# Performance work log

Measured on AMD Instinct MI355X. Metric: run time of the kernel, lower is better.

## Reference

```python
import jax, jax.numpy as jnp
import numpy as np

EPS = 1e-6
SLOPE = 0.25  # nn.PReLU() default init, recreated each forward -> constant slope


def conv_norm(x, W, b, g, beta):
    # 1x1 conv: [B,C,T,F] x [O,C] -> [B,O,T,F]
    y = jnp.einsum('bctf,oc->botf', x, W) + b[None, :, None, None]
    # GroupNorm(num_groups=1): normalize over (C,T,F) per sample
    mu = jnp.mean(y, axis=(1, 2, 3), keepdims=True)
    var = jnp.var(y, axis=(1, 2, 3), keepdims=True)
    y = (y - mu) * jax.lax.rsqrt(var + EPS)
    y = y * g[None, :, None, None] + beta[None, :, None, None]
    # PReLU with constant slope 0.25
    return jnp.where(y >= 0, y, SLOPE * y)


def setup_inputs() -> dict:
    key = jax.random.key(0)
    ks = jax.random.split(key, 16)
    B, C, T, F = 2, 256, 512, 128
    N, H = 4, 64
    CN = C // N
    f32 = jnp.float32

    def w(k, shape, fan_in):
        return jax.random.normal(k, shape, f32) / np.sqrt(fan_in).astype(np.float32)

    return {
        'x': jax.random.normal(ks[0], (B, C, T, F), f32),
        'Wq': w(ks[1], (N, H, C), C), 'bq': jnp.zeros((N, H), f32),
        'gq': jnp.ones((N, H), f32), 'betaq': jnp.zeros((N, H), f32),
        'Wk': w(ks[2], (N, H, C), C), 'bk': jnp.zeros((N, H), f32),
        'gk': jnp.ones((N, H), f32), 'betak': jnp.zeros((N, H), f32),
        'Wv': w(ks[3], (N, CN, C), C), 'bv': jnp.zeros((N, CN), f32),
        'gv': jnp.ones((N, CN), f32), 'betav': jnp.zeros((N, CN), f32),
        'Wp': w(ks[4], (C, C), C), 'bp': jnp.zeros((C,), f32),
        'gp': jnp.ones((C,), f32), 'betap': jnp.zeros((C,), f32),
    }


def reference(x, Wq, bq, gq, betaq, Wk, bk, gk, betak, Wv, bv, gv, betav,
              Wp, bp, gp, betap):
    B, C, T, F = x.shape
    N = Wq.shape[0]
    CN = C // N

    branch = jax.vmap(conv_norm, in_axes=(None, 0, 0, 0, 0))  # over N heads

    def to_seq(y):
        # [N,B,H,T,F] -> transpose(1,2) in torch -> [N,B,T,H,F] -> flatten(2)
        return jnp.swapaxes(y, 2, 3).reshape(y.shape[0], y.shape[1], y.shape[3], -1)

    Q = to_seq(branch(x, Wq, bq, gq, betaq))  # [N,B,T,H*F]
    K = to_seq(branch(x, Wk, bk, gk, betak))  # [N,B,T,H*F]
    V = to_seq(branch(x, Wv, bv, gv, betav))  # [N,B,T,CN*F]

    scale = 1.0 / np.sqrt(Q.shape[-1]).astype(np.float32)
    attn = jax.nn.softmax(jnp.einsum('nbtd,nbsd->nbts', Q, K) * scale, axis=-1)
    Vo = jnp.einsum('nbts,nbsd->nbtd', attn, V)  # [N,B,T,CN*F]

    # exact replication of the original reshape chain (incl. (f,t) reinterpret)
    Vo = Vo.reshape(N * B, T, CN * F)
    Vo = jnp.swapaxes(Vo, 1, 2)                    # [N*B, CN*F, T]
    Vo = Vo.reshape(N, B, CN, T, F)
    Vo = jnp.swapaxes(Vo, 0, 1).reshape(B, C, T, F)

    out = conv_norm(Vo, Wp, bp, gp, betap)
    return out + x
```

## Files before the change

kernel.cpp:

```cpp
#include <hip/hip_runtime.h>
#include <cstddef>

typedef unsigned short u16;

typedef __bf16 bf16x8 __attribute__((ext_vector_type(8)));
typedef float  f32x4  __attribute__((ext_vector_type(4)));
typedef short  s16x8  __attribute__((ext_vector_type(8)));

__device__ __forceinline__ float us2f(u16 u){
  unsigned int w = ((unsigned int)u) << 16; float f; __builtin_memcpy(&f,&w,4); return f;
}
__device__ __forceinline__ u16 f2us(float f){
  unsigned int u; __builtin_memcpy(&u,&f,4);
  u = (u + 0x7FFFu + ((u>>16)&1u)) >> 16;
  return (u16)u;
}

__device__ __forceinline__ f32x4 mfma16(bf16x8 a, bf16x8 b, f32x4 c){
  return __builtin_amdgcn_mfma_f32_16x16x32_bf16(a, b, c, 0, 0, 0);
}
__device__ __forceinline__ ushort4 pack4(f32x4 a){
  ushort4 p; p.x=f2us(a[0]); p.y=f2us(a[1]); p.z=f2us(a[2]); p.w=f2us(a[3]); return p;
}

constexpr int CC=256, CT=512, CF=128, CD=8192, CTF=65536;
constexpr float EPSV = 1e-6f;
constexpr float SLOPEV = 0.25f;
constexpr float QSCALE = 0.011048543456039806f;

#define OW_Q 0
#define OB_Q 65536
#define OG_Q 65792
#define OBE_Q 66048
#define OW_K 66304
#define OB_K 131840
#define OG_K 132096
#define OBE_K 132352
#define OW_V 132608
#define OB_V 198144
#define OG_V 198400
#define OBE_V 198656
#define OW_P 198912
#define OB_P 264448
#define OG_P 264704
#define OBE_P 264960

__global__ void k_detect(const u16* gq_raw, int* flagp){
  if (threadIdx.x==0 && blockIdx.x==0) *flagp = (gq_raw[0]==0x3F80) ? 1 : 0;
}

__global__ __launch_bounds__(256) void k_prep(
    const void* p1,const void* p2,const void* p3,const void* p4,
    const void* p5,const void* p6,const void* p7,const void* p8,
    const void* p9,const void* p10,const void* p11,const void* p12,
    const void* p13,const void* p14,const void* p15,const void* p16,
    u16* dst, const int* flagp)
{
  const void* src; int size; int off;
  switch(blockIdx.y){
    case  0: src=p1;  size=65536; off=OW_Q;  break;
    case  1: src=p2;  size=256;   off=OB_Q;  break;
    case  2: src=p3;  size=256;   off=OG_Q;  break;
    case  3: src=p4;  size=256;   off=OBE_Q; break;
    case  4: src=p5;  size=65536; off=OW_K;  break;
    case  5: src=p6;  size=256;   off=OB_K;  break;
    case  6: src=p7;  size=256;   off=OG_K;  break;
    case  7: src=p8;  size=256;   off=OBE_K; break;
    case  8: src=p9;  size=65536; off=OW_V;  break;
    case  9: src=p10; size=256;   off=OB_V;  break;
    case 10: src=p11; size=256;   off=OG_V;  break;
    case 11: src=p12; size=256;   off=OBE_V; break;
    case 12: src=p13; size=65536; off=OW_P;  break;
    case 13: src=p14; size=256;   off=OB_P;  break;
    case 14: src=p15; size=256;   off=OG_P;  break;
    default: src=p16; size=256;   off=OBE_P; break;
  }
  int idx = blockIdx.x*256 + threadIdx.x;
  if (idx >= size) return;
  u16 v;
  if (*flagp) v = ((const u16*)src)[idx];
  else        v = f2us(((const float*)src)[idx]);
  dst[off+idx] = v;
}

__global__ __launch_bounds__(256) void k_conv(
    const void* x, const u16* wtsb,
    u16* qn, u16* kn, u16* vn,
    float* stats, const int* flagp, int n, int b0)
{
  const int tid = threadIdx.x;
  const int tf0 = blockIdx.x * 64;
  const int flag = *flagp;

  __shared__ __align__(16) u16 Xs[64][264];
  __shared__ float wred[3][4][2];

  {
    const int tfl = (tid & 31) * 2;
    const int cb  = (tid >> 5) * 4;
    if (flag){
      const u16* xq = (const u16*)x + (size_t)b0*CC*CTF + tf0 + tfl;
      #pragma unroll
      for (int p=0;p<8;p++){
        int c0 = p*32 + cb;
        u16 a0[4], a1[4];
        #pragma unroll
        for (int i=0;i<4;i++){
          ushort2 u = *(const ushort2*)&xq[(size_t)(c0+i)*CTF];
          a0[i]=u.x; a1[i]=u.y;
        }
        *(ushort4*)&Xs[tfl][c0]   = *(const ushort4*)a0;
        *(ushort4*)&Xs[tfl+1][c0] = *(const ushort4*)a1;
      }
    } else {
      const float* xq = (const float*)x + (size_t)b0*CC*CTF + tf0 + tfl;
      #pragma unroll
      for (int p=0;p<8;p++){
        int c0 = p*32 + cb;
        u16 a0[4], a1[4];
        #pragma unroll
        for (int i=0;i<4;i++){
          float2 u = *(const float2*)&xq[(size_t)(c0+i)*CTF];
          a0[i]=f2us(u.x); a1[i]=f2us(u.y);
        }
        *(ushort4*)&Xs[tfl][c0]   = *(const ushort4*)a0;
        *(ushort4*)&Xs[tfl+1][c0] = *(const ushort4*)a1;
      }
    }
  }
  __syncthreads();

  const int l  = tid & 63, w = tid >> 6;
  const int lr = l & 15,  kg = l >> 4;
  const int wy = w >> 1,  wx = w & 1;
  const u16* arow0 = &Xs[wy*32 + lr][8*kg];
  const u16* arow1 = &Xs[wy*32 + 16 + lr][8*kg];
  const int t  = tf0 >> 7;
  const int fb = (tf0 & 127) + wy*32 + 4*kg;
  const int o0 = wx*32 + lr;

  for (int br=0; br<3; ++br){
    const u16* W    = wtsb + (br==0?OW_Q: br==1?OW_K:OW_V) + n*64*256;
    const u16* bias = wtsb + (br==0?OB_Q: br==1?OB_K:OB_V) + n*64;
    u16* yo = (br==0? qn : (br==1? kn : vn));
    const u16* bp0 = W + o0*256 + 8*kg;
    const u16* bp1 = bp0 + 16*256;
    float bb0 = us2f(bias[o0]);
    float bb1 = us2f(bias[o0+16]);
    f32x4 acc00 = {bb0,bb0,bb0,bb0};
    f32x4 acc01 = {bb1,bb1,bb1,bb1};
    f32x4 acc10 = {bb0,bb0,bb0,bb0};
    f32x4 acc11 = {bb1,bb1,bb1,bb1};
    #pragma unroll
    for (int d=0; d<256; d+=32){
      bf16x8 a0 = *(const bf16x8*)(arow0 + d);
      bf16x8 a1 = *(const bf16x8*)(arow1 + d);
      bf16x8 b0 = *(const bf16x8*)(bp0 + d);
      bf16x8 b1 = *(const bf16x8*)(bp1 + d);
      acc00 = mfma16(a0,b0,acc00);
      acc01 = mfma16(a0,b1,acc01);
      acc10 = mfma16(a1,b0,acc10);
      acc11 = mfma16(a1,b1,acc11);
    }
    float s=0.f, s2=0.f;
    #pragma unroll
    for (int ii=0; ii<4; ++ii){
      float v;
      v=acc00[ii]; s+=v; s2+=v*v;
      v=acc01[ii]; s+=v; s2+=v*v;
      v=acc10[ii]; s+=v; s2+=v*v;
      v=acc11[ii]; s+=v; s2+=v*v;
    }
    #pragma unroll
    for (int m=1; m<64; m<<=1){ s += __shfl_xor(s,m); s2 += __shfl_xor(s2,m); }
    if (l==0){ wred[br][w][0]=s; wred[br][w][1]=s2; }
    const size_t ybase = (size_t)t*CD + fb;
    *(ushort4*)&yo[ybase + (size_t)o0*CF]           = pack4(acc00);
    *(ushort4*)&yo[ybase + (size_t)(o0+16)*CF]      = pack4(acc01);
    *(ushort4*)&yo[ybase + 16 + (size_t)o0*CF]      = pack4(acc10);
    *(ushort4*)&yo[ybase + 16 + (size_t)(o0+16)*CF] = pack4(acc11);
  }
  __syncthreads();
  if (tid < 3){
    float s  = wred[tid][0][0]+wred[tid][1][0]+wred[tid][2][0]+wred[tid][3][0];
    float s2 = wred[tid][0][1]+wred[tid][1][1]+wred[tid][2][1]+wred[tid][3][1];
    int g = tid*8 + n*2 + b0;
    atomicAdd(&stats[2*g],   s);
    atomicAdd(&stats[2*g+1], s2);
  }
}

__global__ __launch_bounds__(256) void k_norm(
    u16* q, u16* k, u16* v, const u16* wtsb,
    const float* stats, int n, int b0)
{
  const int br = blockIdx.y;
  u16* y = (br==0? q : (br==1? k : v));
  const u16* g  = wtsb + (br==0?OG_Q : br==1?OG_K :OG_V ) + n*64;
  const u16* be = wtsb + (br==0?OBE_Q: br==1?OBE_K:OBE_V) + n*64;
  size_t idx0 = ((size_t)blockIdx.x*256 + threadIdx.x)*8;
  int ch = (int)((idx0 >> 7) & 63);
  int grp = br*8 + n*2 + b0;
  float sm = stats[2*grp], sq = stats[2*grp+1];
  const float Minv = 1.0f/4194304.0f;
  float mean = sm*Minv;
  float var  = fmaxf(sq*Minv - mean*mean, 0.0f);
  float rs = rsqrtf(var + EPSV);
  float gg = us2f(g[ch]) * rs;
  float bb = us2f(be[ch]);
  float sc = (br==0)? QSCALE : 1.0f;
  ushort4 u0 = *(const ushort4*)&y[idx0];
  ushort4 u1 = *(const ushort4*)&y[idx0+4];
  float vals[8] = {us2f(u0.x),us2f(u0.y),us2f(u0.z),us2f(u0.w),
                   us2f(u1.x),us2f(u1.y),us2f(u1.z),us2f(u1.w)};
  #pragma unroll
  for (int j=0;j<8;j++){
    float t = (vals[j]-mean)*gg + bb;
    t = (t>=0.f)? t : SLOPEV*t;
    vals[j] = t*sc;
  }
  ushort4 o0, o1;
  o0.x=f2us(vals[0]); o0.y=f2us(vals[1]); o0.z=f2us(vals[2]); o0.w=f2us(vals[3]);
  o1.x=f2us(vals[4]); o1.y=f2us(vals[5]); o1.z=f2us(vals[6]); o1.w=f2us(vals[7]);
  *(ushort4*)&y[idx0]   = o0;
  *(ushort4*)&y[idx0+4] = o1;
}

__global__ __launch_bounds__(512) void k_qk(const u16* __restrict__ qm,
                                            const u16* __restrict__ km,
                                            float* __restrict__ S)
{
  const int tid = threadIdx.x;
  const int l   = tid & 63;
  const int w   = tid >> 6;
  const int lr  = l & 15;
  const int kg  = l >> 4;
  const int s0  = blockIdx.x*32;
  const int t0  = blockIdx.y*32;

  const u16* qp = qm + (size_t)(t0 + lr)*CD + w*1024 + 8*kg;
  const u16* kp = km + (size_t)(s0 + lr)*CD + w*1024 + 8*kg;

  f32x4 acc00 = {0.f,0.f,0.f,0.f};
  f32x4 acc01 = acc00, acc10 = acc00, acc11 = acc00;

  #pragma unroll 4
  for (int d=0; d<1024; d+=32){
    bf16x8 a0 = *(const bf16x8*)(qp + d);
    bf16x8 a1 = *(const bf16x8*)(qp + d + 16*CD);
    bf16x8 b0 = *(const bf16x8*)(kp + d);
    bf16x8 b1 = *(const bf16x8*)(kp + d + 16*CD);
    acc00 = mfma16(a0, b0, acc00);
    acc01 = mfma16(a0, b1, acc01);
    acc10 = mfma16(a1, b0, acc10);
    acc11 = mfma16(a1, b1, acc11);
  }

  __shared__ float Sb[8][32][36];
  #pragma unroll
  for (int ii=0; ii<4; ++ii){
    Sb[w][4*kg+ii][lr]       = acc00[ii];
    Sb[w][4*kg+ii][lr+16]    = acc01[ii];
    Sb[w][16+4*kg+ii][lr]    = acc10[ii];
    Sb[w][16+4*kg+ii][lr+16] = acc11[ii];
  }
  __syncthreads();
  #pragma unroll
  for (int rep=0; rep<2; ++rep){
    int idx = tid + rep*512;
    int tt = idx >> 5, ss = idx & 31;
    float v = 0.f;
    #pragma unroll
    for (int ww=0; ww<8; ++ww) v += Sb[ww][tt][ss];
    S[(size_t)(t0+tt)*CT + s0 + ss] = v;
  }
}

__global__ __launch_bounds__(256) void k_vt(const u16* __restrict__ v,
                                            u16* __restrict__ vt)
{
  __shared__ u16 T[64][72];
  const int tid = threadIdx.x;
  const int d0 = blockIdx.x*64, s0 = blockIdx.y*64;
  {
    int r = tid >> 3, c8 = (tid & 7)*8;
    *(s16x8*)&T[r][c8]    = *(const s16x8*)&v[(size_t)(s0+r)*CD    + d0 + c8];
    *(s16x8*)&T[r+32][c8] = *(const s16x8*)&v[(size_t)(s0+r+32)*CD + d0 + c8];
  }
  __syncthreads();
  int dd = tid >> 2, s16i = (tid & 3)*16;
  u16 tmp[16];
  #pragma unroll
  for (int j=0;j<16;j++) tmp[j] = T[s16i+j][dd];
  *(s16x8*)&vt[(size_t)(d0+dd)*CT + s0 + s16i]     = *(const s16x8*)&tmp[0];
  *(s16x8*)&vt[(size_t)(d0+dd)*CT + s0 + s16i + 8] = *(const s16x8*)&tmp[8];
}

__global__ __launch_bounds__(256) void k_softmax(const float* S, u16* P)
{
  const int row = blockIdx.x;
  const int tid = threadIdx.x;
  const float* Sr = S + (size_t)row*CT;
  u16* Pr = P + (size_t)row*1024;
  float a = Sr[tid], c = Sr[tid+256];
  __shared__ float buf[256];
  float m = fmaxf(a,c);
  buf[tid] = m;
  __syncthreads();
  for (int w=128; w; w>>=1){
    if (tid<w) buf[tid] = fmaxf(buf[tid], buf[tid+w]);
    __syncthreads();
  }
  m = buf[0];
  __syncthreads();
  float e0 = __expf(a-m), e1 = __expf(c-m);
  buf[tid] = e0+e1;
  __syncthreads();
  for (int w=128; w; w>>=1){
    if (tid<w) buf[tid] += buf[tid+w];
    __syncthreads();
  }
  float r = 1.0f/buf[0];
  Pr[tid]     = f2us(e0*r);
  Pr[tid+256] = f2us(e1*r);
}

__device__ __forceinline__ void pv_store(u16* vof, int n, int b0, int dv, int t, float val){
  int cn = dv >> 7, f = dv & 127;
  vof[((size_t)(b0*CC + n*64 + cn))*CTF + (size_t)f*CT + t] = f2us(val);
}

__global__ __launch_bounds__(256) void k_pv(const u16* __restrict__ P,
                                            const u16* __restrict__ vt,
                                            u16* out_u16, u16* vof_ws,
                                            const int* flagp, int n, int b0)
{
  const int tid = threadIdx.x;
  const int l   = tid & 63;
  const int w   = tid >> 6;
  const int lr  = l & 15;
  const int kg  = l >> 4;
  const int dvb = blockIdx.x*64 + (w >> 1)*32;
  const int tb  = blockIdx.y*64 + (w & 1)*32;

  const u16* ap = vt + (size_t)(dvb + lr)*CT + 8*kg;
  const u16* bp = P  + (size_t)(tb  + lr)*1024 + 8*kg;

  f32x4 acc00 = {0.f,0.f,0.f,0.f};
  f32x4 acc01 = acc00, acc10 = acc00, acc11 = acc00;

  #pragma unroll 2
  for (int s=0; s<CT; s+=32){
    bf16x8 a0 = *(const bf16x8*)(ap + s);
    bf16x8 a1 = *(const bf16x8*)(ap + s + 16*CT);
    bf16x8 b0 = *(const bf16x8*)(bp + s);
    bf16x8 b1 = *(const bf16x8*)(bp + s + 16*1024);
    acc00 = mfma16(a0, b0, acc00);
    acc01 = mfma16(a0, b1, acc01);
    acc10 = mfma16(a1, b0, acc10);
    acc11 = mfma16(a1, b1, acc11);
  }

  u16* vof = (*flagp) ? out_u16 : vof_ws;
  const int tA = tb + lr, tB = tA + 16;
  #pragma unroll
  for (int ii=0; ii<4; ++ii){
    int dvA = dvb + 4*kg + ii;
    int dvB = dvA + 16;
    pv_store(vof, n, b0, dvA, tA, acc00[ii]);
    pv_store(vof, n, b0, dvA, tB, acc01[ii]);
    pv_store(vof, n, b0, dvB, tA, acc10[ii]);
    pv_store(vof, n, b0, dvB, tB, acc11[ii]);
  }
}

__global__ __launch_bounds__(256) void k_proj(u16* out_u16, u16* vof_ws,
                                              const int* flagp,
                                              const u16* wtsb,
                                              float* stats)
{
  const int tid = threadIdx.x;
  const int tf0 = blockIdx.x*64;
  const int b   = blockIdx.y;
  u16* xb = ((*flagp) ? out_u16 : vof_ws) + (size_t)b*CC*CTF;

  __shared__ __align__(16) u16 Xs[64][264];
  __shared__ float wred[4][2];

  {
    const int tfl = (tid & 31) * 2;
    const int cb  = (tid >> 5) * 4;
    const u16* xq = xb + tf0 + tfl;
    #pragma unroll
    for (int p=0;p<8;p++){
      int c0 = p*32 + cb;
      u16 a0[4], a1[4];
      #pragma unroll
      for (int i=0;i<4;i++){
        ushort2 u = *(const ushort2*)&xq[(size_t)(c0+i)*CTF];
        a0[i]=u.x; a1[i]=u.y;
      }
      *(ushort4*)&Xs[tfl][c0]   = *(const ushort4*)a0;
      *(ushort4*)&Xs[tfl+1][c0] = *(const ushort4*)a1;
    }
  }
  __syncthreads();

  const int l  = tid & 63, w = tid >> 6;
  const int lr = l & 15,  kg = l >> 4;
  const int wy = w >> 1,  wx = w & 1;
  const u16* arow0 = &Xs[wy*32 + lr][8*kg];
  const u16* arow1 = &Xs[wy*32 + 16 + lr][8*kg];
  const size_t sb = (size_t)tf0 + wy*32 + 4*kg;
  float ts=0.f, ts2=0.f;

  for (int oc=0; oc<4; ++oc){
    const int o0 = oc*64 + wx*32 + lr;
    const u16* bp0 = wtsb + OW_P + o0*256 + 8*kg;
    const u16* bp1 = bp0 + 16*256;
    float bb0 = us2f(wtsb[OB_P + o0]);
    float bb1 = us2f(wtsb[OB_P + o0 + 16]);
    f32x4 acc00 = {bb0,bb0,bb0,bb0};
    f32x4 acc01 = {bb1,bb1,bb1,bb1};
    f32x4 acc10 = {bb0,bb0,bb0,bb0};
    f32x4 acc11 = {bb1,bb1,bb1,bb1};
    #pragma unroll
    for (int d=0; d<256; d+=32){
      bf16x8 a0 = *(const bf16x8*)(arow0 + d);
      bf16x8 a1 = *(const bf16x8*)(arow1 + d);
      bf16x8 b0 = *(const bf16x8*)(bp0 + d);
      bf16x8 b1 = *(const bf16x8*)(bp1 + d);
      acc00 = mfma16(a0,b0,acc00);
      acc01 = mfma16(a0,b1,acc01);
      acc10 = mfma16(a1,b0,acc10);
      acc11 = mfma16(a1,b1,acc11);
    }
    #pragma unroll
    for (int ii=0; ii<4; ++ii){
      float v;
      v=acc00[ii]; ts+=v; ts2+=v*v;
      v=acc01[ii]; ts+=v; ts2+=v*v;
      v=acc10[ii]; ts+=v; ts2+=v*v;
      v=acc11[ii]; ts+=v; ts2+=v*v;
    }
    *(ushort4*)&xb[(size_t)o0*CTF + sb]           = pack4(acc00);
    *(ushort4*)&xb[(size_t)(o0+16)*CTF + sb]      = pack4(acc01);
    *(ushort4*)&xb[(size_t)o0*CTF + sb + 16]      = pack4(acc10);
    *(ushort4*)&xb[(size_t)(o0+16)*CTF + sb + 16] = pack4(acc11);
  }
  #pragma unroll
  for (int m=1; m<64; m<<=1){ ts += __shfl_xor(ts,m); ts2 += __shfl_xor(ts2,m); }
  if (l==0){ wred[w][0]=ts; wred[w][1]=ts2; }
  __syncthreads();
  if (tid==0){
    float s  = wred[0][0]+wred[1][0]+wred[2][0]+wred[3][0];
    float s2 = wred[0][1]+wred[1][1]+wred[2][1]+wred[3][1];
    atomicAdd(&stats[2*(24+b)],   s);
    atomicAdd(&stats[2*(24+b)+1], s2);
  }
}

__global__ __launch_bounds__(256) void k_final(void* dout, const void* x,
                                               const u16* vof_ws, const int* flagp,
                                               const u16* wtsb,
                                               const float* stats)
{
  const int flag = *flagp;
  size_t idx0 = ((size_t)blockIdx.x*256 + threadIdx.x)*8;
  int b = (int)(idx0 >> 24);
  int c = (int)((idx0 >> 16) & 255);
  float sm = stats[2*(24+b)], sq = stats[2*(24+b)+1];
  const float Minv = 1.0f/16777216.0f;
  float mean = sm*Minv;
  float var  = fmaxf(sq*Minv - mean*mean, 0.0f);
  float rs = rsqrtf(var + EPSV);
  float gg = us2f(wtsb[OG_P + c])*rs, bb = us2f(wtsb[OBE_P + c]);

  const u16* yp = flag ? (const u16*)dout : vof_ws;
  ushort4 u0 = *(const ushort4*)&yp[idx0];
  ushort4 u1 = *(const ushort4*)&yp[idx0+4];
  float vy[8] = {us2f(u0.x),us2f(u0.y),us2f(u0.z),us2f(u0.w),
                 us2f(u1.x),us2f(u1.y),us2f(u1.z),us2f(u1.w)};
  float vx[8];
  if (flag){
    const u16* xb = (const u16*)x;
    ushort4 x0 = *(const ushort4*)&xb[idx0];
    ushort4 x1 = *(const ushort4*)&xb[idx0+4];
    vx[0]=us2f(x0.x); vx[1]=us2f(x0.y); vx[2]=us2f(x0.z); vx[3]=us2f(x0.w);
    vx[4]=us2f(x1.x); vx[5]=us2f(x1.y); vx[6]=us2f(x1.z); vx[7]=us2f(x1.w);
  } else {
    const float* xf = (const float*)x;
    float4 x0 = *(const float4*)&xf[idx0];
    float4 x1 = *(const float4*)&xf[idx0+4];
    vx[0]=x0.x; vx[1]=x0.y; vx[2]=x0.z; vx[3]=x0.w;
    vx[4]=x1.x; vx[5]=x1.y; vx[6]=x1.z; vx[7]=x1.w;
  }
  #pragma unroll
  for (int j=0;j<8;j++){
    float t = (vy[j]-mean)*gg + bb;
    t = (t>=0.f)? t : SLOPEV*t;
    vy[j] = t + vx[j];
  }
  if (flag){
    u16* ob = (u16*)dout;
    ushort4 o0, o1;
    o0.x=f2us(vy[0]); o0.y=f2us(vy[1]); o0.z=f2us(vy[2]); o0.w=f2us(vy[3]);
    o1.x=f2us(vy[4]); o1.y=f2us(vy[5]); o1.z=f2us(vy[6]); o1.w=f2us(vy[7]);
    *(ushort4*)&ob[idx0]   = o0;
    *(ushort4*)&ob[idx0+4] = o1;
  } else {
    float* of = (float*)dout;
    *(float4*)&of[idx0]   = make_float4(vy[0],vy[1],vy[2],vy[3]);
    *(float4*)&of[idx0+4] = make_float4(vy[4],vy[5],vy[6],vy[7]);
  }
}

extern "C" void kernel_launch(void* const* d_in, const int* in_sizes, int n_in,
                              void* d_out, int out_size, void* d_ws, size_t ws_size,
                              hipStream_t stream)
{
  (void)in_sizes; (void)n_in; (void)out_size; (void)ws_size;
  char* ws = (char*)d_ws;
  int* flagp    = (int*)ws;
  float* stats  = (float*)(ws + 16);
  u16* wtsb     = (u16*)(ws + 512);
  u16* qn       = (u16*)(ws + 532480);
  u16* kn       = (u16*)(ws + 8921088);
  u16* vn       = (u16*)(ws + 17309696);
  float* Sn     = (float*)(ws + 25698304);
  u16* vof_ws   = (u16*)(ws + 27262976);
  u16* out_u16  = (u16*)d_out;

  hipMemsetAsync(stats, 0, 256, stream);
  k_detect<<<1,64,0,stream>>>((const u16*)d_in[3], flagp);
  k_prep<<<dim3(256,16),256,0,stream>>>(d_in[1],d_in[2],d_in[3],d_in[4],
                                        d_in[5],d_in[6],d_in[7],d_in[8],
                                        d_in[9],d_in[10],d_in[11],d_in[12],
                                        d_in[13],d_in[14],d_in[15],d_in[16],
                                        wtsb, flagp);
  for (int n=0; n<4; ++n){
    for (int b0=0; b0<2; ++b0){
      k_conv<<<dim3(1024),256,0,stream>>>(d_in[0], wtsb, qn,kn,vn, stats, flagp, n, b0);
      k_norm<<<dim3(2048,3),256,0,stream>>>(qn,kn,vn, wtsb, stats, n, b0);
      k_qk<<<dim3(16,16),512,0,stream>>>(qn,kn,Sn);
      k_vt<<<dim3(128,8),256,0,stream>>>(vn, qn);
      k_softmax<<<512,256,0,stream>>>(Sn,(u16*)Sn);
      k_pv<<<dim3(128,8),256,0,stream>>>((const u16*)Sn, qn, out_u16, vof_ws, flagp, n, b0);
    }
  }
  k_proj<<<dim3(1024,2),256,0,stream>>>(out_u16, vof_ws, flagp, wtsb, stats);
  k_final<<<16384,256,0,stream>>>(d_out, d_in[0], vof_ws, flagp, wtsb, stats);
}
```

Baseline: 1.535 ms.

## Coalesce conv/pv/proj stores via LDS staging and fuse V norm into transpose

Conv, PV and projection kernels now stage their MFMA output tiles in shared memory and write them out as contiguous 16-element vectors, instead of scattered 4-element or single-element stores. The V-branch GroupNorm+PReLU moves out of k_norm into the transpose kernel, which saves one full read/write pass over V. The aim is to cut uncoalesced global writes, especially the PV kernel's per-element strided stores. The cost is extra __syncthreads and shared-memory use in each kernel.

```diff
diff --git a/kernel.cpp b/kernel.cpp
--- a/kernel.cpp
+++ b/kernel.cpp
@@ -93,6 +93,7 @@
   const int flag = *flagp;
 
   __shared__ __align__(16) u16 Xs[64][264];
+  __shared__ __align__(16) u16 Ys[64][72];
   __shared__ float wred[3][4][2];
 
   {
@@ -135,8 +136,9 @@
   const int wy = w >> 1,  wx = w & 1;
   const u16* arow0 = &Xs[wy*32 + lr][8*kg];
   const u16* arow1 = &Xs[wy*32 + 16 + lr][8*kg];
-  const int t  = tf0 >> 7;
-  const int fb = (tf0 & 127) + wy*32 + 4*kg;
+  const int t   = tf0 >> 7;
+  const int f0g = tf0 & 127;
+  const size_t ybase = (size_t)t*CD + f0g;
   const int o0 = wx*32 + lr;
 
   for (int br=0; br<3; ++br){
@@ -174,13 +176,20 @@
     #pragma unroll
     for (int m=1; m<64; m<<=1){ s += __shfl_xor(s,m); s2 += __shfl_xor(s2,m); }
     if (l==0){ wred[br][w][0]=s; wred[br][w][1]=s2; }
-    const size_t ybase = (size_t)t*CD + fb;
-    *(ushort4*)&yo[ybase + (size_t)o0*CF]           = pack4(acc00);
-    *(ushort4*)&yo[ybase + (size_t)(o0+16)*CF]      = pack4(acc01);
-    *(ushort4*)&yo[ybase + 16 + (size_t)o0*CF]      = pack4(acc10);
-    *(ushort4*)&yo[ybase + 16 + (size_t)(o0+16)*CF] = pack4(acc11);
-  }
-  __syncthreads();
+    __syncthreads();
+    *(ushort4*)&Ys[wx*32 + lr][wy*32 + 4*kg]           = pack4(acc00);
+    *(ushort4*)&Ys[wx*32 + 16 + lr][wy*32 + 4*kg]      = pack4(acc01);
+    *(ushort4*)&Ys[wx*32 + lr][wy*32 + 16 + 4*kg]      = pack4(acc10);
+    *(ushort4*)&Ys[wx*32 + 16 + lr][wy*32 + 16 + 4*kg] = pack4(acc11);
+    __syncthreads();
+    {
+      int oo = tid >> 2, sg = (tid & 3)*16;
+      size_t adr = ybase + (size_t)oo*CF + sg;
+      *(s16x8*)&yo[adr]     = *(const s16x8*)&Ys[oo][sg];
+      *(s16x8*)&yo[adr + 8] = *(const s16x8*)&Ys[oo][sg + 8];
+    }
+    __syncthreads();
+  }
   if (tid < 3){
     float s  = wred[tid][0][0]+wred[tid][1][0]+wred[tid][2][0]+wred[tid][3][0];
     float s2 = wred[tid][0][1]+wred[tid][1][1]+wred[tid][2][1]+wred[tid][3][1];
@@ -191,13 +200,13 @@
 }
 
 __global__ __launch_bounds__(256) void k_norm(
-    u16* q, u16* k, u16* v, const u16* wtsb,
+    u16* q, u16* k, const u16* wtsb,
     const float* stats, int n, int b0)
 {
   const int br = blockIdx.y;
-  u16* y = (br==0? q : (br==1? k : v));
-  const u16* g  = wtsb + (br==0?OG_Q : br==1?OG_K :OG_V ) + n*64;
-  const u16* be = wtsb + (br==0?OBE_Q: br==1?OBE_K:OBE_V) + n*64;
+  u16* y = (br==0? q : k);
+  const u16* g  = wtsb + (br==0?OG_Q : OG_K ) + n*64;
+  const u16* be = wtsb + (br==0?OBE_Q: OBE_K) + n*64;
   size_t idx0 = ((size_t)blockIdx.x*256 + threadIdx.x)*8;
   int ch = (int)((idx0 >> 7) & 63);
   int grp = br*8 + n*2 + b0;
@@ -276,8 +285,10 @@
   }
 }
 
-__global__ __launch_bounds__(256) void k_vt(const u16* __restrict__ v,
-                                            u16* __restrict__ vt)
+__global__ __launch_bounds__(256) void k_vtn(const u16* __restrict__ v,
+                                             u16* __restrict__ vt,
+                                             const u16* wtsb,
+                                             const float* stats, int n, int b0)
 {
   __shared__ u16 T[64][72];
   const int tid = threadIdx.x;
@@ -289,9 +300,23 @@
   }
   __syncthreads();
   int dd = tid >> 2, s16i = (tid & 3)*16;
+  int ch = (d0 + dd) >> 7;
+  int grp = 16 + n*2 + b0;
+  float sm = stats[2*grp], sq = stats[2*grp+1];
+  const float Minv = 1.0f/4194304.0f;
+  float mean = sm*Minv;
+  float var  = fmaxf(sq*Minv - mean*mean, 0.0f);
+  float rs = rsqrtf(var + EPSV);
+  float gg = us2f(wtsb[OG_V  + n*64 + ch]) * rs;
+  float bb = us2f(wtsb[OBE_V + n*64 + ch]);
   u16 tmp[16];
   #pragma unroll
-  for (int j=0;j<16;j++) tmp[j] = T[s16i+j][dd];
+  for (int j=0;j<16;j++){
+    float val = us2f(T[s16i+j][dd]);
+    float t = (val-mean)*gg + bb;
+    t = (t>=0.f)? t : SLOPEV*t;
+    tmp[j] = f2us(t);
+  }
   *(s16x8*)&vt[(size_t)(d0+dd)*CT + s0 + s16i]     = *(const s16x8*)&tmp[0];
   *(s16x8*)&vt[(size_t)(d0+dd)*CT + s0 + s16i + 8] = *(const s16x8*)&tmp[8];
 }
@@ -325,11 +350,6 @@
   Pr[tid+256] = f2us(e1*r);
 }
 
-__device__ __forceinline__ void pv_store(u16* vof, int n, int b0, int dv, int t, float val){
-  int cn = dv >> 7, f = dv & 127;
-  vof[((size_t)(b0*CC + n*64 + cn))*CTF + (size_t)f*CT + t] = f2us(val);
-}
-
 __global__ __launch_bounds__(256) void k_pv(const u16* __restrict__ P,
                                             const u16* __restrict__ vt,
                                             u16* out_u16, u16* vof_ws,
@@ -340,11 +360,13 @@
   const int w   = tid >> 6;
   const int lr  = l & 15;
   const int kg  = l >> 4;
-  const int dvb = blockIdx.x*64 + (w >> 1)*32;
-  const int tb  = blockIdx.y*64 + (w & 1)*32;
-
-  const u16* ap = vt + (size_t)(dvb + lr)*CT + 8*kg;
-  const u16* bp = P  + (size_t)(tb  + lr)*1024 + 8*kg;
+  const int dv0 = blockIdx.x*64;
+  const int t00 = blockIdx.y*64;
+  const int dvofs = (w >> 1)*32;
+  const int tofs  = (w & 1)*32;
+
+  const u16* ap = P  + (size_t)(t00 + tofs + lr)*1024 + 8*kg;
+  const u16* bp = vt + (size_t)(dv0 + dvofs + lr)*CT  + 8*kg;
 
   f32x4 acc00 = {0.f,0.f,0.f,0.f};
   f32x4 acc01 = acc00, acc10 = acc00, acc11 = acc00;
@@ -352,25 +374,30 @@
   #pragma unroll 2
   for (int s=0; s<CT; s+=32){
     bf16x8 a0 = *(const bf16x8*)(ap + s);
-    bf16x8 a1 = *(const bf16x8*)(ap + s + 16*CT);
+    bf16x8 a1 = *(const bf16x8*)(ap + s + 16*1024);
     bf16x8 b0 = *(const bf16x8*)(bp + s);
-    bf16x8 b1 = *(const bf16x8*)(bp + s + 16*1024);
+    bf16x8 b1 = *(const bf16x8*)(bp + s + 16*CT);
     acc00 = mfma16(a0, b0, acc00);
     acc01 = mfma16(a0, b1, acc01);
     acc10 = mfma16(a1, b0, acc10);
     acc11 = mfma16(a1, b1, acc11);
   }
 
+  __shared__ __align__(16) u16 Ot[64][72];
+  *(ushort4*)&Ot[dvofs + lr][tofs + 4*kg]           = pack4(acc00);
+  *(ushort4*)&Ot[dvofs + 16 + lr][tofs + 4*kg]      = pack4(acc01);
+  *(ushort4*)&Ot[dvofs + lr][tofs + 16 + 4*kg]      = pack4(acc10);
+  *(ushort4*)&Ot[dvofs + 16 + lr][tofs + 16 + 4*kg] = pack4(acc11);
+  __syncthreads();
+
   u16* vof = (*flagp) ? out_u16 : vof_ws;
-  const int tA = tb + lr, tB = tA + 16;
-  #pragma unroll
-  for (int ii=0; ii<4; ++ii){
-    int dvA = dvb + 4*kg + ii;
-    int dvB = dvA + 16;
-    pv_store(vof, n, b0, dvA, tA, acc00[ii]);
-    pv_store(vof, n, b0, dvA, tB, acc01[ii]);
-    pv_store(vof, n, b0, dvB, tA, acc10[ii]);
-    pv_store(vof, n, b0, dvB, tB, acc11[ii]);
+  {
+    int r = tid >> 2, sg = (tid & 3)*16;
+    int dv = dv0 + r;
+    int cn = dv >> 7, f = dv & 127;
+    size_t adr = ((size_t)(b0*CC + n*64 + cn))*CTF + (size_t)f*CT + t00 + sg;
+    *(s16x8*)&vof[adr]     = *(const s16x8*)&Ot[r][sg];
+    *(s16x8*)&vof[adr + 8] = *(const s16x8*)&Ot[r][sg + 8];
   }
 }
 
@@ -385,6 +412,7 @@
   u16* xb = ((*flagp) ? out_u16 : vof_ws) + (size_t)b*CC*CTF;
 
   __shared__ __align__(16) u16 Xs[64][264];
+  __shared__ __align__(16) u16 Yp[64][72];
   __shared__ float wred[4][2];
 
   {
@@ -411,11 +439,11 @@
   const int wy = w >> 1,  wx = w & 1;
   const u16* arow0 = &Xs[wy*32 + lr][8*kg];
   const u16* arow1 = &Xs[wy*32 + 16 + lr][8*kg];
-  const size_t sb = (size_t)tf0 + wy*32 + 4*kg;
   float ts=0.f, ts2=0.f;
 
   for (int oc=0; oc<4; ++oc){
-    const int o0 = oc*64 + wx*32 + lr;
+    const int o0c = oc*64;
+    const int o0  = o0c + wx*32 + lr;
     const u16* bp0 = wtsb + OW_P + o0*256 + 8*kg;
     const u16* bp1 = bp0 + 16*256;
     float bb0 = us2f(wtsb[OB_P + o0]);
@@ -443,10 +471,19 @@
       v=acc10[ii]; ts+=v; ts2+=v*v;
       v=acc11[ii]; ts+=v; ts2+=v*v;
     }
-    *(ushort4*)&xb[(size_t)o0*CTF + sb]           = pack4(acc00);
-    *(ushort4*)&xb[(size_t)(o0+16)*CTF + sb]      = pack4(acc01);
-    *(ushort4*)&xb[(size_t)o0*CTF + sb + 16]      = pack4(acc10);
-    *(ushort4*)&xb[(size_t)(o0+16)*CTF + sb + 16] = pack4(acc11);
+    __syncthreads();
+    *(ushort4*)&Yp[wx*32 + lr][wy*32 + 4*kg]           = pack4(acc00);
+    *(ushort4*)&Yp[wx*32 + 16 + lr][wy*32 + 4*kg]      = pack4(acc01);
+    *(ushort4*)&Yp[wx*32 + lr][wy*32 + 16 + 4*kg]      = pack4(acc10);
+    *(ushort4*)&Yp[wx*32 + 16 + lr][wy*32 + 16 + 4*kg] = pack4(acc11);
+    __syncthreads();
+    {
+      int ol = tid >> 2, sg = (tid & 3)*16;
+      size_t adr = (size_t)(o0c + ol)*CTF + tf0 + sg;
+      *(s16x8*)&xb[adr]     = *(const s16x8*)&Yp[ol][sg];
+      *(s16x8*)&xb[adr + 8] = *(const s16x8*)&Yp[ol][sg + 8];
+    }
+    __syncthreads();
   }
   #pragma unroll
   for (int m=1; m<64; m<<=1){ ts += __shfl_xor(ts,m); ts2 += __shfl_xor(ts2,m); }
@@ -541,9 +578,9 @@
   for (int n=0; n<4; ++n){
     for (int b0=0; b0<2; ++b0){
       k_conv<<<dim3(1024),256,0,stream>>>(d_in[0], wtsb, qn,kn,vn, stats, flagp, n, b0);
-      k_norm<<<dim3(2048,3),256,0,stream>>>(qn,kn,vn, wtsb, stats, n, b0);
+      k_norm<<<dim3(2048,2),256,0,stream>>>(qn,kn, wtsb, stats, n, b0);
       k_qk<<<dim3(16,16),512,0,stream>>>(qn,kn,Sn);
-      k_vt<<<dim3(128,8),256,0,stream>>>(vn, qn);
+      k_vtn<<<dim3(128,8),256,0,stream>>>(vn, qn, wtsb, stats, n, b0);
       k_softmax<<<512,256,0,stream>>>(Sn,(u16*)Sn);
       k_pv<<<dim3(128,8),256,0,stream>>>((const u16*)Sn, qn, out_u16, vof_ws, flagp, n, b0);
     }
```

After: 1.525 ms. About the same (-0.7%).
